# Kernel tuning notes

Hardware: AMD Instinct MI355X
Metric: run time of the kernel (lower is better)

The kernel has to match this reference:

```python
import jax, jax.numpy as jnp
import numpy as np

FINE_RES = 128      # fine grid resolution per axis
POOL = 2            # kernel_size == stride == 2
COARSE_RES = FINE_RES // POOL  # 64


def setup_inputs() -> dict:
    key = jax.random.key(0)
    kf, kc = jax.random.split(key)
    N, C = 1000000, 64
    features = jax.random.normal(kf, (N, C), dtype=jnp.float32)
    coords = jax.random.randint(kc, (N, 3), 0, FINE_RES, dtype=jnp.int32)
    num_segments = COARSE_RES ** 3  # 262144 coarse voxels (dense linearization)
    return {"features": features, "coords": coords, "num_segments": num_segments}


def reference(features, coords, num_segments):
    # Sparse 3D max pool with kernel==stride==2: each fine voxel maps to
    # exactly one coarse voxel floor(ijk / 2); reduce by segment max.
    cc = coords // POOL  # [N,3] coarse ijk
    seg = (cc[:, 0] * COARSE_RES + cc[:, 1]) * COARSE_RES + cc[:, 2]  # [N] linear coarse id
    pooled = jax.ops.segment_max(features, seg, num_segments=num_segments)  # [S,C]
    # fvdb fills uncovered coarse voxels with -inf; module masks inf -> 0
    pooled = jnp.where(jnp.isinf(pooled), jnp.zeros((), pooled.dtype), pooled)
    return pooled
```

## Files before the change

kernel.cpp:

```cpp
#include <hip/hip_runtime.h>
#include <math.h>


#define CHANNELS 64
#define COARSE_RES 64
#define NSEG (COARSE_RES * COARSE_RES * COARSE_RES)
#define CAP 16
#define MAXOVF 65536
#define SPW 8

__global__ void zero_kernel(int* __restrict__ buf, int n) {
    int i = blockIdx.x * blockDim.x + threadIdx.x;
    int stride = gridDim.x * blockDim.x;
    for (; i < n; i += stride) buf[i] = 0;
}

__global__ void scatter_kernel(const int* __restrict__ coords,
                               int* __restrict__ cursor,
                               int* __restrict__ ovf,
                               int* __restrict__ indices,
                               int n) {
    int p = blockIdx.x * blockDim.x + threadIdx.x;
    if (p >= n) return;
    int ci = coords[3 * p + 0] >> 1;
    int cj = coords[3 * p + 1] >> 1;
    int ck = coords[3 * p + 2] >> 1;
    int seg = (ci * COARSE_RES + cj) * COARSE_RES + ck;
    int pos = atomicAdd(&cursor[seg], 1);
    if (pos < CAP) {
        indices[seg * CAP + pos] = p;
    } else {
        int o = atomicAdd(&ovf[0], 1);
        if (o < MAXOVF) {
            ovf[16 + 2 * o + 0] = p;
            ovf[16 + 2 * o + 1] = seg;
        }
    }
}

__global__ __launch_bounds__(256) void gather_strip_kernel(
        const float* __restrict__ feat,
        const int* __restrict__ indices,
        const int* __restrict__ cursor,
        float* __restrict__ out) {
    int wave = (blockIdx.x * blockDim.x + threadIdx.x) >> 6;
    int lane = threadIdx.x & 63;
    long segbase = (long)wave * SPW;

    int cnt_l = 0;
    if (lane < SPW) {
        cnt_l = cursor[segbase + lane];
        if (cnt_l > CAP) cnt_l = CAP;
    }
    int2 idx2 = reinterpret_cast<const int2*>(indices + segbase * CAP)[lane];

    int s = 0, t = 0, cs = 0;
    float m = -INFINITY;

    #define SKIP_EMPTIES()                                         \
        for (;;) {                                                 \
            if (s >= SPW) break;                                   \
            cs = __shfl(cnt_l, s);                                 \
            if (cs > 0) break;                                     \
            out[(segbase + s) * CHANNELS + lane] = 0.0f;           \
            ++s;                                                   \
        }

    #define EXTRACT(r, dst) {                                      \
        int lsrc = (s << 3) + ((r) >> 1);                          \
        int lo_ = __shfl(idx2.x, lsrc);                            \
        int hi_ = __shfl(idx2.y, lsrc);                            \
        dst = ((r) & 1) ? hi_ : lo_; }

    #define ISSUE(F0, F1, F2, F3, FLUSH, SEG) {                    \
        int r0_ = t;                                               \
        int r1_ = min(t + 1, cs - 1);                              \
        int r2_ = min(t + 2, cs - 1);                              \
        int r3_ = min(t + 3, cs - 1);                              \
        int p0_, p1_, p2_, p3_;                                    \
        EXTRACT(r0_, p0_); EXTRACT(r1_, p1_);                      \
        EXTRACT(r2_, p2_); EXTRACT(r3_, p3_);                      \
        F0 = feat[(long)p0_ * CHANNELS + lane];                    \
        F1 = feat[(long)p1_ * CHANNELS + lane];                    \
        F2 = feat[(long)p2_ * CHANNELS + lane];                    \
        F3 = feat[(long)p3_ * CHANNELS + lane];                    \
        t += 4;                                                    \
        FLUSH = (t >= cs); SEG = s;                                \
        if (FLUSH) { ++s; t = 0; SKIP_EMPTIES(); } }

    #define CONSUME(F0, F1, F2, F3, FLUSH, SEG) {                  \
        m = fmaxf(m, fmaxf(fmaxf(F0, F1), fmaxf(F2, F3)));         \
        if (FLUSH) {                                               \
            out[(segbase + SEG) * CHANNELS + lane] = m;            \
            m = -INFINITY; } }

    SKIP_EMPTIES();
    float fA0, fA1, fA2, fA3, fB0, fB1, fB2, fB3;
    bool flA = false, flB = false;
    int sgA = 0, sgB = 0;
    bool haveA = false, haveB = false;
    if (s < SPW) { ISSUE(fA0, fA1, fA2, fA3, flA, sgA); haveA = true; }
    if (s < SPW) { ISSUE(fB0, fB1, fB2, fB3, flB, sgB); haveB = true; }
    while (haveA) {
        CONSUME(fA0, fA1, fA2, fA3, flA, sgA); haveA = false;
        if (s < SPW) { ISSUE(fA0, fA1, fA2, fA3, flA, sgA); haveA = true; }
        if (!haveB) { if (!haveA) break; else continue; }
        CONSUME(fB0, fB1, fB2, fB3, flB, sgB); haveB = false;
        if (s < SPW) { ISSUE(fB0, fB1, fB2, fB3, flB, sgB); haveB = true; }
    }
    #undef SKIP_EMPTIES
    #undef EXTRACT
    #undef ISSUE
    #undef CONSUME
}

__global__ void overflow_kernel(const float* __restrict__ feat,
                                const int* __restrict__ ovf,
                                float* __restrict__ out) {
    int n = min(ovf[0], MAXOVF);
    int total = n * CHANNELS;
    int stride = gridDim.x * blockDim.x;
    for (int k = blockIdx.x * blockDim.x + threadIdx.x; k < total; k += stride) {
        int e = k >> 6;
        int c = k & 63;
        int p = ovf[16 + 2 * e + 0];
        int seg = ovf[16 + 2 * e + 1];
        float v = feat[(long)p * CHANNELS + c];
        int* addr = (int*)&out[(long)seg * CHANNELS + c];
        int old = *addr;
        while (__int_as_float(old) < v) {
            int assumed = old;
            old = atomicCAS(addr, assumed, __float_as_int(v));
            if (old == assumed) break;
        }
    }
}

extern "C" void kernel_launch(void* const* d_in, const int* in_sizes, int n_in,
                              void* d_out, int out_size, void* d_ws, size_t ws_size,
                              hipStream_t stream) {
    const float* feat = (const float*)d_in[0];
    const int* coords = (const int*)d_in[1];
    int npoints = in_sizes[0] / CHANNELS;

    int* cursor  = (int*)d_ws;
    int* ovf     = cursor + NSEG;
    int* indices = ovf + 16 + 2 * MAXOVF;

    const int BLOCK = 256;

    zero_kernel<<<512, BLOCK, 0, stream>>>(cursor, NSEG + 16);

    int grid_pts = (npoints + BLOCK - 1) / BLOCK;
    scatter_kernel<<<grid_pts, BLOCK, 0, stream>>>(coords, cursor, ovf, indices, npoints);

    int grid_gather = NSEG / (SPW * (BLOCK / 64));
    gather_strip_kernel<<<grid_gather, BLOCK, 0, stream>>>(feat, indices, cursor, (float*)d_out);

    overflow_kernel<<<16, BLOCK, 0, stream>>>(feat, ovf, (float*)d_out);
}
```

Measured before the change: 140.5 us.

## Vectorize gather with float4 row-groups and triple-buffer feature loads

The gather kernel now splits each 64-lane wave into four 16-lane groups. Each group loads one whole 256-byte feature row with float4 loads, where before every lane issued four scalar loads across four rows. Partial maxima from the four groups are merged with xor-shuffles when a segment is flushed, and only 16 lanes write the result as float4. The software pipeline also goes from two buffers to three, keeping more loads in flight. This cuts load instruction count and raises memory-level parallelism, at the cost of extra shuffles per segment and more involved tail handling.

```diff
diff --git a/kernel.cpp b/kernel.cpp
--- a/kernel.cpp
+++ b/kernel.cpp
@@ -45,7 +45,11 @@
         float* __restrict__ out) {
     int wave = (blockIdx.x * blockDim.x + threadIdx.x) >> 6;
     int lane = threadIdx.x & 63;
+    int g = lane >> 4;
+    int q = lane & 15;
     long segbase = (long)wave * SPW;
+    const float4* feat4 = reinterpret_cast<const float4*>(feat);
+    float4* out4 = reinterpret_cast<float4*>(out);
 
     int cnt_l = 0;
     if (lane < SPW) {
@@ -55,61 +59,78 @@
     int2 idx2 = reinterpret_cast<const int2*>(indices + segbase * CAP)[lane];
 
     int s = 0, t = 0, cs = 0;
-    float m = -INFINITY;
+    const float4 Z4 = make_float4(0.f, 0.f, 0.f, 0.f);
+    const float4 NEG4 = make_float4(-INFINITY, -INFINITY, -INFINITY, -INFINITY);
+    float4 m = NEG4;
 
     #define SKIP_EMPTIES()                                         \
         for (;;) {                                                 \
             if (s >= SPW) break;                                   \
             cs = __shfl(cnt_l, s);                                 \
             if (cs > 0) break;                                     \
-            out[(segbase + s) * CHANNELS + lane] = 0.0f;           \
+            if (lane < 16) out4[(segbase + s) * 16 + q] = Z4;      \
             ++s;                                                   \
         }
 
-    #define EXTRACT(r, dst) {                                      \
-        int lsrc = (s << 3) + ((r) >> 1);                          \
-        int lo_ = __shfl(idx2.x, lsrc);                            \
-        int hi_ = __shfl(idx2.y, lsrc);                            \
-        dst = ((r) & 1) ? hi_ : lo_; }
-
-    #define ISSUE(F0, F1, F2, F3, FLUSH, SEG) {                    \
-        int r0_ = t;                                               \
-        int r1_ = min(t + 1, cs - 1);                              \
-        int r2_ = min(t + 2, cs - 1);                              \
-        int r3_ = min(t + 3, cs - 1);                              \
-        int p0_, p1_, p2_, p3_;                                    \
-        EXTRACT(r0_, p0_); EXTRACT(r1_, p1_);                      \
-        EXTRACT(r2_, p2_); EXTRACT(r3_, p3_);                      \
-        F0 = feat[(long)p0_ * CHANNELS + lane];                    \
-        F1 = feat[(long)p1_ * CHANNELS + lane];                    \
-        F2 = feat[(long)p2_ * CHANNELS + lane];                    \
-        F3 = feat[(long)p3_ * CHANNELS + lane];                    \
+    #define ISSUE(F, FLUSH, SEG) {                                 \
+        int r_ = t + g;                                            \
+        if (r_ > cs - 1) r_ = cs - 1;                              \
+        int pos_ = (s << 4) + r_;                                  \
+        int lo_ = __shfl(idx2.x, pos_ >> 1);                       \
+        int hi_ = __shfl(idx2.y, pos_ >> 1);                       \
+        int p_ = (pos_ & 1) ? hi_ : lo_;                           \
+        F = feat4[(long)p_ * 16 + q];                              \
         t += 4;                                                    \
         FLUSH = (t >= cs); SEG = s;                                \
         if (FLUSH) { ++s; t = 0; SKIP_EMPTIES(); } }
 
-    #define CONSUME(F0, F1, F2, F3, FLUSH, SEG) {                  \
-        m = fmaxf(m, fmaxf(fmaxf(F0, F1), fmaxf(F2, F3)));         \
+    #define CONSUME(F, FLUSH, SEG) {                               \
+        m.x = fmaxf(m.x, F.x); m.y = fmaxf(m.y, F.y);              \
+        m.z = fmaxf(m.z, F.z); m.w = fmaxf(m.w, F.w);              \
         if (FLUSH) {                                               \
-            out[(segbase + SEG) * CHANNELS + lane] = m;            \
-            m = -INFINITY; } }
+            m.x = fmaxf(m.x, __shfl_xor(m.x, 16));                 \
+            m.y = fmaxf(m.y, __shfl_xor(m.y, 16));                 \
+            m.z = fmaxf(m.z, __shfl_xor(m.z, 16));                 \
+            m.w = fmaxf(m.w, __shfl_xor(m.w, 16));                 \
+            m.x = fmaxf(m.x, __shfl_xor(m.x, 32));                 \
+            m.y = fmaxf(m.y, __shfl_xor(m.y, 32));                 \
+            m.z = fmaxf(m.z, __shfl_xor(m.z, 32));                 \
+            m.w = fmaxf(m.w, __shfl_xor(m.w, 32));                 \
+            if (lane < 16) out4[(segbase + SEG) * 16 + q] = m;     \
+            m = NEG4; } }
 
     SKIP_EMPTIES();
-    float fA0, fA1, fA2, fA3, fB0, fB1, fB2, fB3;
-    bool flA = false, flB = false;
-    int sgA = 0, sgB = 0;
-    bool haveA = false, haveB = false;
-    if (s < SPW) { ISSUE(fA0, fA1, fA2, fA3, flA, sgA); haveA = true; }
-    if (s < SPW) { ISSUE(fB0, fB1, fB2, fB3, flB, sgB); haveB = true; }
-    while (haveA) {
-        CONSUME(fA0, fA1, fA2, fA3, flA, sgA); haveA = false;
-        if (s < SPW) { ISSUE(fA0, fA1, fA2, fA3, flA, sgA); haveA = true; }
-        if (!haveB) { if (!haveA) break; else continue; }
-        CONSUME(fB0, fB1, fB2, fB3, flB, sgB); haveB = false;
-        if (s < SPW) { ISSUE(fB0, fB1, fB2, fB3, flB, sgB); haveB = true; }
+    float4 A, B, C;
+    bool flA = false, flB = false, flC = false;
+    int sgA = 0, sgB = 0, sgC = 0;
+    bool hA = false, hB = false, hC = false;
+
+    if (s < SPW) { ISSUE(A, flA, sgA); hA = true; }
+    if (s < SPW) { ISSUE(B, flB, sgB); hB = true; }
+    if (s < SPW) { ISSUE(C, flC, sgC); hC = true; }
+
+    for (;;) {
+        if (!hA) break;
+        CONSUME(A, flA, sgA); hA = false;
+        if (s < SPW) { ISSUE(A, flA, sgA); hA = true; }
+        if (!hB) break;
+        CONSUME(B, flB, sgB); hB = false;
+        if (s < SPW) { ISSUE(B, flB, sgB); hB = true; }
+        if (!hC) break;
+        CONSUME(C, flC, sgC); hC = false;
+        if (s < SPW) { ISSUE(C, flC, sgC); hC = true; }
+    }
+    if (!hA) {
+        if (hB) CONSUME(B, flB, sgB);
+        if (hC) CONSUME(C, flC, sgC);
+    } else if (!hB) {
+        if (hC) CONSUME(C, flC, sgC);
+        CONSUME(A, flA, sgA);
+    } else {
+        CONSUME(A, flA, sgA);
+        CONSUME(B, flB, sgB);
     }
     #undef SKIP_EMPTIES
-    #undef EXTRACT
     #undef ISSUE
     #undef CONSUME
 }
```

New measurement: 142.0 us. No clear change (+1.1%).
